# Optimization experiments

Hardware: AMD Instinct MI355X
Metric: run time of the kernel (lower is better)

The kernel has to match this reference:

```python
import jax, jax.numpy as jnp
import numpy as np

DIM = 64
NUM_NODES = 64
SEQ_LEN = 256
BATCH = 64


def setup_inputs() -> dict:
    key = jax.random.key(0)
    ks = jax.random.split(key, 8)
    D = DIM
    x = jax.random.normal(ks[0], (SEQ_LEN, BATCH, NUM_NODES, D), dtype=jnp.float32)
    mask = jnp.ones((SEQ_LEN,), dtype=jnp.int32)
    # msg MLP: Linear(3D -> D) + GELU
    lim_msg = 1.0 / np.sqrt(3 * D)
    msg_W = jax.random.uniform(ks[1], (D, 3 * D), minval=-lim_msg, maxval=lim_msg, dtype=jnp.float32)
    msg_b = jax.random.uniform(ks[2], (D,), minval=-lim_msg, maxval=lim_msg, dtype=jnp.float32)
    # GRUCell(input=D, hidden=D); torch init U(-1/sqrt(hidden), 1/sqrt(hidden))
    lim_g = 1.0 / np.sqrt(D)
    W_ih = jax.random.uniform(ks[3], (3 * D, D), minval=-lim_g, maxval=lim_g, dtype=jnp.float32)
    W_hh = jax.random.uniform(ks[4], (3 * D, D), minval=-lim_g, maxval=lim_g, dtype=jnp.float32)
    b_ih = jax.random.uniform(ks[5], (3 * D,), minval=-lim_g, maxval=lim_g, dtype=jnp.float32)
    b_hh = jax.random.uniform(ks[6], (3 * D,), minval=-lim_g, maxval=lim_g, dtype=jnp.float32)
    # TimeEncode params
    basis_freq = jnp.asarray(1.0 / 10.0 ** np.linspace(0, 9, D), dtype=jnp.float32)
    phase = jnp.zeros((D,), dtype=jnp.float32)
    return {"x": x, "mask": mask, "msg_W": msg_W, "msg_b": msg_b,
            "W_ih": W_ih, "W_hh": W_hh, "b_ih": b_ih, "b_hh": b_hh,
            "basis_freq": basis_freq, "phase": phase}


def _forward(x, mask, msg_W, msg_b, W_ih, W_hh, b_ih, b_hh, basis_freq, phase):
    T, B, C, D = x.shape
    # TimeEncode: cos(t * freq + phase) -> [T, D]
    ts = jnp.arange(T, dtype=jnp.float32)[:, None]
    t_enc = jnp.cos(ts * basis_freq[None, :] + phase[None, :])
    # init_func == 'mean': mean over time -> [B, C, D] -> [B*C, D]
    s0 = jnp.mean(x, axis=0).reshape(B * C, D)
    # time_range = arange(T) * mask (gather indices)
    tr = jnp.arange(T) * mask.astype(jnp.int32)
    x_seq = x[tr].reshape(T, B * C, D)      # gathered timesteps
    te_seq = t_enc[tr]                       # [T, D]

    def step(s, inp):
        xt, tt = inp                        # xt: [B*C, D], tt: [D]
        tt_b = jnp.broadcast_to(tt[None, :], xt.shape)
        cat = jnp.concatenate([xt, s, tt_b], axis=-1)  # [B*C, 3D]
        msg = jax.nn.gelu(cat @ msg_W.T + msg_b, approximate=False)
        # GRUCell (torch gate order: r, z, n)
        gi = msg @ W_ih.T + b_ih
        gh = s @ W_hh.T + b_hh
        i_r, i_z, i_n = jnp.split(gi, 3, axis=-1)
        h_r, h_z, h_n = jnp.split(gh, 3, axis=-1)
        r = jax.nn.sigmoid(i_r + h_r)
        z = jax.nn.sigmoid(i_z + h_z)
        n = jnp.tanh(i_n + r * h_n)
        s_new = (1.0 - z) * n + z * s
        return s_new, s_new

    _, states = jax.lax.scan(step, s0, (x_seq, te_seq))
    return states.reshape(T, B, C, D)


def reference(x, mask, msg_W, msg_b, W_ih, W_hh, b_ih, b_hh, basis_freq, phase):
    return _forward(x, mask, msg_W, msg_b, W_ih, W_hh, b_ih, b_hh, basis_freq, phase)
```

## Files before the change

### kernel.cpp

```cpp
#include <hip/hip_runtime.h>
#include <math.h>

#define DD    64
#define TT    256
#define NROW  4096
#define BLK   512
#define GRID  256

typedef __attribute__((ext_vector_type(8))) short  short8;
typedef __attribute__((ext_vector_type(4))) float  f32x4;

#define BARRIER() do {                                        \
    asm volatile("s_waitcnt lgkmcnt(0)" ::: "memory");        \
    __builtin_amdgcn_sched_barrier(0);                        \
    __builtin_amdgcn_s_barrier();                             \
    __builtin_amdgcn_sched_barrier(0);                        \
  } while (0)

__device__ __forceinline__ unsigned short f2bf(float f) {
  unsigned u = __builtin_bit_cast(unsigned, f);
  u += 0x7fffu + ((u >> 16) & 1u);
  return (unsigned short)(u >> 16);
}

__device__ __forceinline__ unsigned long long pack4(f32x4 v) {
  return (unsigned long long)f2bf(v[0])
       | ((unsigned long long)f2bf(v[1]) << 16)
       | ((unsigned long long)f2bf(v[2]) << 32)
       | ((unsigned long long)f2bf(v[3]) << 48);
}

__device__ __forceinline__ short8 pack_frag(f32x4 a, f32x4 b) {
  short8 r;
  r[0] = (short)f2bf(a[0]); r[1] = (short)f2bf(a[1]);
  r[2] = (short)f2bf(a[2]); r[3] = (short)f2bf(a[3]);
  r[4] = (short)f2bf(b[0]); r[5] = (short)f2bf(b[1]);
  r[6] = (short)f2bf(b[2]); r[7] = (short)f2bf(b[3]);
  return r;
}

__device__ __forceinline__ short8 load_wfrag(const float* p) {
  f32x4 a = *(const f32x4*)p;
  f32x4 b = *(const f32x4*)(p + 4);
  return pack_frag(a, b);
}

__device__ __forceinline__ float fsigmoid(float x) {
  return __builtin_amdgcn_rcpf(1.0f + __expf(-x));
}
__device__ __forceinline__ float ftanh(float x) {
  return 1.0f - 2.0f * __builtin_amdgcn_rcpf(1.0f + __expf(2.0f * x));
}
__device__ __forceinline__ float ferf(float x) {
  float ax = fabsf(x);
  float t  = __builtin_amdgcn_rcpf(fmaf(0.3275911f, ax, 1.0f));
  float p  = fmaf(1.061405429f, t, -1.453152027f);
  p = fmaf(p, t, 1.421413741f);
  p = fmaf(p, t, -0.284496736f);
  p = fmaf(p, t, 0.254829592f);
  p = p * t;
  float y = 1.0f - p * __expf(-ax * ax);
  return copysignf(y, x);
}

__global__ void bias_kernel(const float* __restrict__ msg_W,
                            const float* __restrict__ msg_b,
                            const float* __restrict__ freq,
                            const float* __restrict__ phase,
                            float* __restrict__ bias_t) {
  __shared__ float teL[DD];
  const int t = blockIdx.x;
  const int j = threadIdx.x;
  teL[j] = cosf(fmaf((float)t, freq[j], phase[j]));
  __syncthreads();
  float acc = msg_b[j];
  const float* wrow = msg_W + j * 192 + 128;
  #pragma unroll 8
  for (int k = 0; k < DD; ++k) acc = fmaf(teL[k], wrow[k], acc);
  bias_t[t * DD + j] = acc;
}

__launch_bounds__(BLK, 1)
__global__ void scan7(const float* __restrict__ x,
                      const int*   __restrict__ mask,
                      const float* __restrict__ msg_W,
                      const float* __restrict__ W_ih,
                      const float* __restrict__ W_hh,
                      const float* __restrict__ b_ih,
                      const float* __restrict__ b_hh,
                      const float* __restrict__ bias_t,
                      float* __restrict__ out) {
  __shared__ alignas(16) unsigned short ss[16 * 72];
  __shared__ alignas(16) unsigned short ms[16 * 72];
  __shared__ alignas(16) float amxl[64 * 20];
  __shared__ alignas(16) float ghl[16 * 260];
  __shared__ alignas(16) float s0a[16 * 68];
  __shared__ int tr_lds[TT];

  const int tid  = threadIdx.x;
  const int lane = tid & 63;
  const int wv   = tid >> 6;
  const int grp  = wv >> 2;
  const int w4   = wv & 3;
  const int col  = lane & 15;
  const int kh   = lane >> 4;
  const int n    = w4 * 16 + col;
  const int row0 = blockIdx.x * 16;

  if (tid < TT) tr_lds[tid] = tid * mask[tid];

  short8 ws[2], wi[3][2], wh[3][2], wx[2];
  float bsum01[2] = {0.f, 0.f}, bih2 = 0.f, bhh2 = 0.f;
  if (grp == 0) {
    const float* mrow = msg_W + (size_t)n * 192;
    ws[0] = load_wfrag(mrow + 64 + kh * 8);
    ws[1] = load_wfrag(mrow + 96 + kh * 8);
    #pragma unroll
    for (int p = 0; p < 3; ++p) {
      const float* irow = W_ih + (size_t)(p * 64 + n) * 64;
      #pragma unroll
      for (int kf = 0; kf < 2; ++kf) wi[p][kf] = load_wfrag(irow + kf * 32 + kh * 8);
    }
    bsum01[0] = b_ih[n]      + b_hh[n];
    bsum01[1] = b_ih[64 + n] + b_hh[64 + n];
    bih2 = b_ih[128 + n];
    bhh2 = b_hh[128 + n];
  } else {
    const float* mrow = msg_W + (size_t)n * 192;
    wx[0] = load_wfrag(mrow + kh * 8);
    wx[1] = load_wfrag(mrow + 32 + kh * 8);
    #pragma unroll
    for (int p = 0; p < 3; ++p) {
      const float* hrow = W_hh + (size_t)(p * 64 + n) * 64;
      #pragma unroll
      for (int kf = 0; kf < 2; ++kf) wh[p][kf] = load_wfrag(hrow + kf * 32 + kh * 8);
    }
  }

  {
    const int half = tid >> 8, rem = tid & 255;
    const int fr = rem >> 4, fd = (rem & 15) * 4;
    const float* px = x + ((size_t)half * 128) * (NROW * DD)
                        + (size_t)(row0 + fr) * DD + fd;
    f32x4 acc = {0.f, 0.f, 0.f, 0.f};
    #pragma unroll 4
    for (int tl = 0; tl < 128; ++tl) {
      f32x4 v = *(const f32x4*)(px + (size_t)tl * (NROW * DD));
      acc += v;
    }
    *(f32x4*)&ghl[tid * 4] = acc;
  }
  __syncthreads();
  if (tid < 256) {
    const int fr = tid >> 4, fd = (tid & 15) * 4;
    f32x4 a = *(const f32x4*)&ghl[tid * 4];
    f32x4 b = *(const f32x4*)&ghl[(256 + tid) * 4];
    f32x4 m = (a + b) * (1.0f / 256.0f);
    *(f32x4*)&s0a[fr * 68 + fd] = m;
    *(unsigned long long*)&ss[fr * 72 + fd] = pack4(m);
  }

  f32x4 xva = {0,0,0,0}, xvb = {0,0,0,0}, xvc = {0,0,0,0}, xvd = {0,0,0,0};
  if (grp == 1) {
    const float* px0 = x + (size_t)(row0 + (lane & 15)) * DD + kh * 8;
    f32x4 f0a = *(const f32x4*)(px0);
    f32x4 f0b = *(const f32x4*)(px0 + 4);
    f32x4 f1a = *(const f32x4*)(px0 + 32);
    f32x4 f1b = *(const f32x4*)(px0 + 36);
    short8 xa0 = pack_frag(f0a, f0b);
    short8 xa1 = pack_frag(f1a, f1b);
    f32x4 c = {0.f, 0.f, 0.f, 0.f};
    c = __builtin_amdgcn_mfma_f32_16x16x32_bf16(xa0, wx[0], c, 0, 0, 0);
    c = __builtin_amdgcn_mfma_f32_16x16x32_bf16(xa1, wx[1], c, 0, 0, 0);
    const float bt = bias_t[n];
    c[0] += bt; c[1] += bt; c[2] += bt; c[3] += bt;
    *(f32x4*)&amxl[n * 20 + kh * 4] = c;
    const float* px1 = x + ((size_t)tr_lds[1] * NROW + row0 + (lane & 15)) * DD + kh * 8;
    xva = *(const f32x4*)(px1);
    xvb = *(const f32x4*)(px1 + 4);
    xvc = *(const f32x4*)(px1 + 32);
    xvd = *(const f32x4*)(px1 + 36);
  }
  __syncthreads();

  float s_reg[4] = {0.f, 0.f, 0.f, 0.f};
  if (grp == 0) {
    #pragma unroll
    for (int i = 0; i < 4; ++i) s_reg[i] = s0a[(kh * 4 + i) * 68 + n];
    __builtin_amdgcn_s_setprio(1);
  }

  const int t1  = tid & 255;
  const int fr1 = t1 >> 4;
  const int fd1 = (t1 & 15) * 4;

  for (int t = 0; t < TT; ++t) {
    if (grp == 0) {
      const unsigned short* as = &ss[(lane & 15) * 72];
      short8 sa0 = *(const short8*)(as + kh * 8);
      short8 sa1 = *(const short8*)(as + 32 + kh * 8);
      f32x4 am4 = *(const f32x4*)&amxl[n * 20 + kh * 4];
      f32x4 ams = {0.f, 0.f, 0.f, 0.f};
      ams = __builtin_amdgcn_mfma_f32_16x16x32_bf16(sa0, ws[0], ams, 0, 0, 0);
      ams = __builtin_amdgcn_mfma_f32_16x16x32_bf16(sa1, ws[1], ams, 0, 0, 0);
      #pragma unroll
      for (int i = 0; i < 4; ++i) {
        float a = ams[i] + am4[i];
        float g = 0.5f * a * (1.0f + ferf(a * 0.70710678118654752f));
        ms[(kh * 4 + i) * 72 + n] = f2bf(g);
      }
    } else {
      const unsigned short* as = &ss[(lane & 15) * 72];
      short8 sa0 = *(const short8*)(as + kh * 8);
      short8 sa1 = *(const short8*)(as + 32 + kh * 8);
      f32x4 agh[3];
      #pragma unroll
      for (int p = 0; p < 3; ++p) {
        f32x4 c = {0.f, 0.f, 0.f, 0.f};
        c = __builtin_amdgcn_mfma_f32_16x16x32_bf16(sa0, wh[p][0], c, 0, 0, 0);
        c = __builtin_amdgcn_mfma_f32_16x16x32_bf16(sa1, wh[p][1], c, 0, 0, 0);
        agh[p] = c;
      }
      #pragma unroll
      for (int i = 0; i < 4; ++i) {
        f32x4 gv = { agh[0][i], agh[1][i], agh[2][i], 0.f };
        *(f32x4*)&ghl[(kh * 4 + i) * 260 + n * 4] = gv;
      }
      if (t > 0) {
        f32x4 ov = *(const f32x4*)&s0a[fr1 * 68 + fd1];
        *(f32x4*)(out + ((size_t)(t - 1) * NROW + row0 + fr1) * DD + fd1) = ov;
      }
    }
    BARRIER();

    if (grp == 0) {
      f32x4 gh4[4];
      #pragma unroll
      for (int i = 0; i < 4; ++i)
        gh4[i] = *(const f32x4*)&ghl[(kh * 4 + i) * 260 + n * 4];
      const unsigned short* am = &ms[(lane & 15) * 72];
      short8 ma0 = *(const short8*)(am + kh * 8);
      short8 ma1 = *(const short8*)(am + 32 + kh * 8);
      f32x4 agi[3];
      #pragma unroll
      for (int p = 0; p < 3; ++p) {
        f32x4 c = {0.f, 0.f, 0.f, 0.f};
        c = __builtin_amdgcn_mfma_f32_16x16x32_bf16(ma0, wi[p][0], c, 0, 0, 0);
        c = __builtin_amdgcn_mfma_f32_16x16x32_bf16(ma1, wi[p][1], c, 0, 0, 0);
        agi[p] = c;
      }
      #pragma unroll
      for (int i = 0; i < 4; ++i) {
        const int rr = kh * 4 + i;
        float gr  = agi[0][i] + gh4[i][0] + bsum01[0];
        float gz  = agi[1][i] + gh4[i][1] + bsum01[1];
        float gni = agi[2][i] + bih2;
        float gnh = gh4[i][2] + bhh2;
        float rg = fsigmoid(gr);
        float zg = fsigmoid(gz);
        float ng = ftanh(fmaf(rg, gnh, gni));
        float sn = fmaf(zg, s_reg[i] - ng, ng);
        s_reg[i] = sn;
        ss[rr * 72 + n]  = f2bf(sn);
        s0a[rr * 68 + n] = sn;
      }
    } else {
      if (t + 1 < TT) {
        float bt = bias_t[tr_lds[t + 1] * DD + n];
        short8 xa0 = pack_frag(xva, xvb);
        short8 xa1 = pack_frag(xvc, xvd);
        f32x4 c = {0.f, 0.f, 0.f, 0.f};
        c = __builtin_amdgcn_mfma_f32_16x16x32_bf16(xa0, wx[0], c, 0, 0, 0);
        c = __builtin_amdgcn_mfma_f32_16x16x32_bf16(xa1, wx[1], c, 0, 0, 0);
        c[0] += bt; c[1] += bt; c[2] += bt; c[3] += bt;
        *(f32x4*)&amxl[n * 20 + kh * 4] = c;
      }
      if (t + 2 < TT) {
        const float* pxn = x + ((size_t)tr_lds[t + 2] * NROW + row0 + (lane & 15)) * DD + kh * 8;
        xva = *(const f32x4*)(pxn);
        xvb = *(const f32x4*)(pxn + 4);
        xvc = *(const f32x4*)(pxn + 32);
        xvd = *(const f32x4*)(pxn + 36);
      }
    }
    BARRIER();
  }

  if (grp == 1) {
    f32x4 ov = *(const f32x4*)&s0a[fr1 * 68 + fd1];
    *(f32x4*)(out + ((size_t)(TT - 1) * NROW + row0 + fr1) * DD + fd1) = ov;
  }
}

extern "C" void kernel_launch(void* const* d_in, const int* in_sizes, int n_in,
                              void* d_out, int out_size, void* d_ws, size_t ws_size,
                              hipStream_t stream) {
  const float* x      = (const float*)d_in[0];
  const int*   mask   = (const int*)  d_in[1];
  const float* msg_W  = (const float*)d_in[2];
  const float* msg_b  = (const float*)d_in[3];
  const float* W_ih   = (const float*)d_in[4];
  const float* W_hh   = (const float*)d_in[5];
  const float* b_ih   = (const float*)d_in[6];
  const float* b_hh   = (const float*)d_in[7];
  const float* freq   = (const float*)d_in[8];
  const float* phase  = (const float*)d_in[9];
  float* out    = (float*)d_out;
  float* bias_t = (float*)d_ws;

  (void)in_sizes; (void)n_in; (void)out_size; (void)ws_size;

  bias_kernel<<<TT, DD, 0, stream>>>(msg_W, msg_b, freq, phase, bias_t);
  scan7<<<GRID, BLK, 0, stream>>>(x, mask, msg_W, W_ih, W_hh,
                                  b_ih, b_hh, bias_t, out);
}
```

Before: 345.3 us.

## Move x-projection MFMA into msg waves and stage bf16 x in LDS

The x·W_msg projection is no longer precomputed by the GRU-hidden wavegroup into an fp32 LDS buffer. Instead, that wavegroup only prefetches the next timestep's x from global memory with coalesced f32x4 loads, packs it to bf16 and writes it to a shared xs tile. The message wavegroup now does all four msg MFMAs itself and carries the time bias in a register. The time loop is unrolled by two with ping-pong x registers. This trims work and LDS traffic on the hidden-state side. The cost is two extra MFMAs per step on the message wavegroup, which sits on the recurrent critical path.

```diff
diff --git a/kernel.cpp b/kernel.cpp
--- a/kernel.cpp
+++ b/kernel.cpp
@@ -81,7 +81,7 @@
 }
 
 __launch_bounds__(BLK, 1)
-__global__ void scan7(const float* __restrict__ x,
+__global__ void scan8(const float* __restrict__ x,
                       const int*   __restrict__ mask,
                       const float* __restrict__ msg_W,
                       const float* __restrict__ W_ih,
@@ -90,11 +90,11 @@
                       const float* __restrict__ b_hh,
                       const float* __restrict__ bias_t,
                       float* __restrict__ out) {
+  __shared__ alignas(16) unsigned short xs[16 * 72];
   __shared__ alignas(16) unsigned short ss[16 * 72];
   __shared__ alignas(16) unsigned short ms[16 * 72];
-  __shared__ alignas(16) float amxl[64 * 20];
+  __shared__ alignas(16) float s0a[16 * 68];
   __shared__ alignas(16) float ghl[16 * 260];
-  __shared__ alignas(16) float s0a[16 * 68];
   __shared__ int tr_lds[TT];
 
   const int tid  = threadIdx.x;
@@ -109,12 +109,12 @@
 
   if (tid < TT) tr_lds[tid] = tid * mask[tid];
 
-  short8 ws[2], wi[3][2], wh[3][2], wx[2];
+  short8 wm[4], wi[3][2], wh[3][2];
   float bsum01[2] = {0.f, 0.f}, bih2 = 0.f, bhh2 = 0.f;
   if (grp == 0) {
     const float* mrow = msg_W + (size_t)n * 192;
-    ws[0] = load_wfrag(mrow + 64 + kh * 8);
-    ws[1] = load_wfrag(mrow + 96 + kh * 8);
+    #pragma unroll
+    for (int kf = 0; kf < 4; ++kf) wm[kf] = load_wfrag(mrow + kf * 32 + kh * 8);
     #pragma unroll
     for (int p = 0; p < 3; ++p) {
       const float* irow = W_ih + (size_t)(p * 64 + n) * 64;
@@ -126,9 +126,6 @@
     bih2 = b_ih[128 + n];
     bhh2 = b_hh[128 + n];
   } else {
-    const float* mrow = msg_W + (size_t)n * 192;
-    wx[0] = load_wfrag(mrow + kh * 8);
-    wx[1] = load_wfrag(mrow + 32 + kh * 8);
     #pragma unroll
     for (int p = 0; p < 3; ++p) {
       const float* hrow = W_hh + (size_t)(p * 64 + n) * 64;
@@ -148,45 +145,28 @@
       f32x4 v = *(const f32x4*)(px + (size_t)tl * (NROW * DD));
       acc += v;
     }
-    *(f32x4*)&ghl[tid * 4] = acc;
+    float* dst = (half == 0) ? &s0a[(rem >> 4) * 68 + fd] : &ghl[rem * 4];
+    *(f32x4*)dst = acc;
   }
   __syncthreads();
   if (tid < 256) {
     const int fr = tid >> 4, fd = (tid & 15) * 4;
-    f32x4 a = *(const f32x4*)&ghl[tid * 4];
-    f32x4 b = *(const f32x4*)&ghl[(256 + tid) * 4];
+    f32x4 a = *(const f32x4*)&s0a[fr * 68 + fd];
+    f32x4 b = *(const f32x4*)&ghl[tid * 4];
     f32x4 m = (a + b) * (1.0f / 256.0f);
     *(f32x4*)&s0a[fr * 68 + fd] = m;
     *(unsigned long long*)&ss[fr * 72 + fd] = pack4(m);
-  }
-
-  f32x4 xva = {0,0,0,0}, xvb = {0,0,0,0}, xvc = {0,0,0,0}, xvd = {0,0,0,0};
-  if (grp == 1) {
-    const float* px0 = x + (size_t)(row0 + (lane & 15)) * DD + kh * 8;
-    f32x4 f0a = *(const f32x4*)(px0);
-    f32x4 f0b = *(const f32x4*)(px0 + 4);
-    f32x4 f1a = *(const f32x4*)(px0 + 32);
-    f32x4 f1b = *(const f32x4*)(px0 + 36);
-    short8 xa0 = pack_frag(f0a, f0b);
-    short8 xa1 = pack_frag(f1a, f1b);
-    f32x4 c = {0.f, 0.f, 0.f, 0.f};
-    c = __builtin_amdgcn_mfma_f32_16x16x32_bf16(xa0, wx[0], c, 0, 0, 0);
-    c = __builtin_amdgcn_mfma_f32_16x16x32_bf16(xa1, wx[1], c, 0, 0, 0);
-    const float bt = bias_t[n];
-    c[0] += bt; c[1] += bt; c[2] += bt; c[3] += bt;
-    *(f32x4*)&amxl[n * 20 + kh * 4] = c;
-    const float* px1 = x + ((size_t)tr_lds[1] * NROW + row0 + (lane & 15)) * DD + kh * 8;
-    xva = *(const f32x4*)(px1);
-    xvb = *(const f32x4*)(px1 + 4);
-    xvc = *(const f32x4*)(px1 + 32);
-    xvd = *(const f32x4*)(px1 + 36);
+    f32x4 xv0 = *(const f32x4*)(x + (size_t)(row0 + fr) * DD + fd);
+    *(unsigned long long*)&xs[fr * 72 + fd] = pack4(xv0);
   }
   __syncthreads();
 
   float s_reg[4] = {0.f, 0.f, 0.f, 0.f};
+  float btc = 0.f;
   if (grp == 0) {
     #pragma unroll
     for (int i = 0; i < 4; ++i) s_reg[i] = s0a[(kh * 4 + i) * 68 + n];
+    btc = bias_t[n];
     __builtin_amdgcn_s_setprio(1);
   }
 
@@ -194,21 +174,33 @@
   const int fr1 = t1 >> 4;
   const int fd1 = (t1 & 15) * 4;
 
-  for (int t = 0; t < TT; ++t) {
+  f32x4 xvA = {0.f, 0.f, 0.f, 0.f}, xvB = {0.f, 0.f, 0.f, 0.f};
+  if (grp == 1)
+    xvA = *(const f32x4*)(x + ((size_t)tr_lds[1] * NROW + row0 + fr1) * DD + fd1);
+
+  auto body = [&](int t, f32x4& xv_use, f32x4& xv_load) {
     if (grp == 0) {
+      const unsigned short* ax = &xs[(lane & 15) * 72];
       const unsigned short* as = &ss[(lane & 15) * 72];
+      short8 xa0 = *(const short8*)(ax + kh * 8);
+      short8 xa1 = *(const short8*)(ax + 32 + kh * 8);
       short8 sa0 = *(const short8*)(as + kh * 8);
       short8 sa1 = *(const short8*)(as + 32 + kh * 8);
-      f32x4 am4 = *(const f32x4*)&amxl[n * 20 + kh * 4];
+      float btn = 0.f;
+      if (t + 1 < TT) btn = bias_t[tr_lds[t + 1] * DD + n];
+      f32x4 amx = {0.f, 0.f, 0.f, 0.f};
+      amx = __builtin_amdgcn_mfma_f32_16x16x32_bf16(xa0, wm[0], amx, 0, 0, 0);
+      amx = __builtin_amdgcn_mfma_f32_16x16x32_bf16(xa1, wm[1], amx, 0, 0, 0);
       f32x4 ams = {0.f, 0.f, 0.f, 0.f};
-      ams = __builtin_amdgcn_mfma_f32_16x16x32_bf16(sa0, ws[0], ams, 0, 0, 0);
-      ams = __builtin_amdgcn_mfma_f32_16x16x32_bf16(sa1, ws[1], ams, 0, 0, 0);
+      ams = __builtin_amdgcn_mfma_f32_16x16x32_bf16(sa0, wm[2], ams, 0, 0, 0);
+      ams = __builtin_amdgcn_mfma_f32_16x16x32_bf16(sa1, wm[3], ams, 0, 0, 0);
       #pragma unroll
       for (int i = 0; i < 4; ++i) {
-        float a = ams[i] + am4[i];
+        float a = amx[i] + ams[i] + btc;
         float g = 0.5f * a * (1.0f + ferf(a * 0.70710678118654752f));
         ms[(kh * 4 + i) * 72 + n] = f2bf(g);
       }
+      btc = btn;
     } else {
       const unsigned short* as = &ss[(lane & 15) * 72];
       short8 sa0 = *(const short8*)(as + kh * 8);
@@ -230,6 +222,8 @@
         f32x4 ov = *(const f32x4*)&s0a[fr1 * 68 + fd1];
         *(f32x4*)(out + ((size_t)(t - 1) * NROW + row0 + fr1) * DD + fd1) = ov;
       }
+      if (t + 2 < TT)
+        xv_load = *(const f32x4*)(x + ((size_t)tr_lds[t + 2] * NROW + row0 + fr1) * DD + fd1);
     }
     BARRIER();
 
@@ -265,25 +259,15 @@
         s0a[rr * 68 + n] = sn;
       }
     } else {
-      if (t + 1 < TT) {
-        float bt = bias_t[tr_lds[t + 1] * DD + n];
-        short8 xa0 = pack_frag(xva, xvb);
-        short8 xa1 = pack_frag(xvc, xvd);
-        f32x4 c = {0.f, 0.f, 0.f, 0.f};
-        c = __builtin_amdgcn_mfma_f32_16x16x32_bf16(xa0, wx[0], c, 0, 0, 0);
-        c = __builtin_amdgcn_mfma_f32_16x16x32_bf16(xa1, wx[1], c, 0, 0, 0);
-        c[0] += bt; c[1] += bt; c[2] += bt; c[3] += bt;
-        *(f32x4*)&amxl[n * 20 + kh * 4] = c;
-      }
-      if (t + 2 < TT) {
-        const float* pxn = x + ((size_t)tr_lds[t + 2] * NROW + row0 + (lane & 15)) * DD + kh * 8;
-        xva = *(const f32x4*)(pxn);
-        xvb = *(const f32x4*)(pxn + 4);
-        xvc = *(const f32x4*)(pxn + 32);
-        xvd = *(const f32x4*)(pxn + 36);
-      }
+      if (t + 1 < TT)
+        *(unsigned long long*)&xs[fr1 * 72 + fd1] = pack4(xv_use);
     }
     BARRIER();
+  };
+
+  for (int tt = 0; tt < TT; tt += 2) {
+    body(tt,     xvA, xvB);
+    body(tt + 1, xvB, xvA);
   }
 
   if (grp == 1) {
@@ -311,6 +295,6 @@
   (void)in_sizes; (void)n_in; (void)out_size; (void)ws_size;
 
   bias_kernel<<<TT, DD, 0, stream>>>(msg_W, msg_b, freq, phase, bias_t);
-  scan7<<<GRID, BLK, 0, stream>>>(x, mask, msg_W, W_ih, W_hh,
+  scan8<<<GRID, BLK, 0, stream>>>(x, mask, msg_W, W_ih, W_hh,
                                   b_ih, b_hh, bias_t, out);
 }
```

Result: faster. 311.3 us (-9.8%).
